# Kernel optimization log

Measured on AMD Instinct MI355X. Metric: run time of the kernel, lower is better.

Reference implementation:

```python
import jax, jax.numpy as jnp
import numpy as np

B, N, DIM, H, DH, M = 4, 1024, 1024, 16, 64, 16  # batch, seq, model dim, heads, head dim, num_mem_kv
QK_SCALE = 10.0  # qk_norm_scale


def l2norm(t, eps=1e-12):
    # F.normalize(t, dim=-1) with clamp_min(eps), groups=1
    n = jnp.linalg.norm(t, axis=-1, keepdims=True)
    return t / jnp.maximum(n, eps)


def rotate_half(x):
    # interleaved pairs: (x0,x1) -> (-x1, x0)
    x = x.reshape(*x.shape[:-1], -1, 2)
    x1, x2 = x[..., 0], x[..., 1]
    return jnp.stack((-x2, x1), axis=-1).reshape(*x.shape[:-2], x.shape[-2] * 2)


def apply_rope(t, freqs):
    # freqs: [n, d], t: [b, h, n, d]
    return t * jnp.cos(freqs) + rotate_half(t) * jnp.sin(freqs)


def setup_inputs() -> dict:
    key = jax.random.key(0)
    ks = jax.random.split(key, 14)
    x = jax.random.normal(ks[0], (B, N, DIM), dtype=jnp.float32)
    # rotary freqs: outer(pos, inv_freq) with each freq repeated twice (interleaved pairs)
    pos = jnp.arange(N, dtype=jnp.float32)
    inv_freq = 1.0 / (10000.0 ** (jnp.arange(0, DH, 2, dtype=jnp.float32) / DH))
    freqs = jnp.repeat(pos[:, None] * inv_freq[None, :], 2, axis=-1)  # [N, DH]
    s = 0.02
    Wq = jax.random.normal(ks[1], (DIM, H * DH), dtype=jnp.float32) * s
    Wk = jax.random.normal(ks[2], (DIM, H * DH), dtype=jnp.float32) * s
    Wv = jax.random.normal(ks[3], (DIM, H * DH), dtype=jnp.float32) * s
    q_scale = 1.0 + 0.1 * jax.random.normal(ks[4], (H, 1, DH), dtype=jnp.float32)
    k_scale = 1.0 + 0.1 * jax.random.normal(ks[5], (H, 1, DH), dtype=jnp.float32)
    mem_k = jax.random.normal(ks[6], (H, M, DH), dtype=jnp.float32)
    mem_v = jax.random.normal(ks[7], (H, M, DH), dtype=jnp.float32)
    W_pre = jnp.eye(H, dtype=jnp.float32) + 0.05 * jax.random.normal(ks[8], (H, H), dtype=jnp.float32)
    W_post = jnp.eye(H, dtype=jnp.float32) + 0.05 * jax.random.normal(ks[9], (H, H), dtype=jnp.float32)
    W_hgate = jax.random.normal(ks[10], (DIM, H), dtype=jnp.float32) * s
    b_hgate = jnp.full((H,), 2.0, dtype=jnp.float32)
    W_vgate = jax.random.normal(ks[11], (DIM, H * DH), dtype=jnp.float32) * s
    b_vgate = jnp.full((H * DH,), 2.0, dtype=jnp.float32)
    Wo = jax.random.normal(ks[12], (H * DH, DIM), dtype=jnp.float32) * s
    return dict(x=x, freqs=freqs, Wq=Wq, Wk=Wk, Wv=Wv, q_scale=q_scale, k_scale=k_scale,
                mem_k=mem_k, mem_v=mem_v, W_pre=W_pre, W_post=W_post,
                W_hgate=W_hgate, b_hgate=b_hgate, W_vgate=W_vgate, b_vgate=b_vgate, Wo=Wo)


def reference(x, freqs, Wq, Wk, Wv, q_scale, k_scale, mem_k, mem_v,
              W_pre, W_post, W_hgate, b_hgate, W_vgate, b_vgate, Wo):
    b, n, _ = x.shape
    # projections -> [b, h, n, dh]
    q = (x @ Wq).reshape(b, n, H, DH).transpose(0, 2, 1, 3)
    k = (x @ Wk).reshape(b, n, H, DH).transpose(0, 2, 1, 3)
    v = (x @ Wv).reshape(b, n, H, DH).transpose(0, 2, 1, 3)
    # qk l2-norm (groups=1) + learned per-head dim scales
    q = l2norm(q) * q_scale
    k = l2norm(k) * k_scale
    # rotary (xpos_scale = None -> scale 1)
    q = apply_rope(q, freqs)
    k = apply_rope(k, freqs)
    # memory key/values, prepended along the kv sequence axis
    mk = (l2norm(mem_k) * k_scale)[None].repeat(b, axis=0)  # [b,h,M,dh]
    mv = mem_v[None].repeat(b, axis=0)
    k = jnp.concatenate((mk, k), axis=-2)  # [b,h,M+n,dh]
    v = jnp.concatenate((mv, v), axis=-2)
    i, j = q.shape[-2], k.shape[-2]
    dots = jnp.einsum('bhid,bhjd->bhij', q, k) * QK_SCALE
    dots = jnp.einsum('bhij,gh->bgij', dots, W_pre)  # pre-softmax talking heads
    # causal mask (memory slots at the front are always visible)
    qpos = jnp.arange(i)
    kpos = jnp.arange(j)
    causal = kpos[None, :] > (qpos[:, None] + (j - i))  # True -> masked
    mask_value = -jnp.finfo(dots.dtype).max
    dots = jnp.where(causal[None, None], mask_value, dots)
    attn = jax.nn.softmax(dots, axis=-1)
    attn = jnp.einsum('bhij,gh->bgij', attn, W_post)  # post-softmax talking heads
    out = jnp.einsum('bhij,bhjd->bhid', attn, v)  # [b,h,n,dh]
    # per-head value gate
    head_gate = jax.nn.sigmoid(x @ W_hgate + b_hgate)  # [b,n,h]
    out = out * head_gate.transpose(0, 2, 1)[..., None]
    out = out.transpose(0, 2, 1, 3).reshape(b, n, H * DH)
    # per-dim value gate (sigmoid)
    out = out * jax.nn.sigmoid(x @ W_vgate + b_vgate)
    return out @ Wo
```

## Files before the change

### kernel.cpp

```cpp
#include <hip/hip_runtime.h>
#include <hip/hip_bf16.h>
#include <cmath>

typedef __attribute__((ext_vector_type(8))) short short8;
typedef __attribute__((ext_vector_type(4))) float f32x4;

__device__ __forceinline__ unsigned short to_bf(float f) {
  __hip_bfloat16 h = __float2bfloat16(f);
  return __builtin_bit_cast(unsigned short, h);
}

__global__ __launch_bounds__(256)
void cvt_bf16x4(const float* __restrict__ in, unsigned short* __restrict__ out, int n4)
{
  int i = blockIdx.x * 256 + threadIdx.x;
  if (i < n4) {
    float4 v = ((const float4*)in)[i];
    ushort4 o;
    o.x = to_bf(v.x); o.y = to_bf(v.y); o.z = to_bf(v.z); o.w = to_bf(v.w);
    ((ushort4*)out)[i] = o;
  }
}

__global__ __launch_bounds__(256)
void transpose_to_bf(const float* __restrict__ W, unsigned short* __restrict__ WT)
{
  __shared__ float tile[64][65];
  const int n0 = blockIdx.x * 64, k0 = blockIdx.y * 64;
  const int t = threadIdx.x, c = t & 63, r4 = t >> 6;
#pragma unroll
  for (int q = 0; q < 16; ++q) {
    int r = (q << 2) + r4;
    tile[r][c] = W[(size_t)(k0 + r) * 1024 + n0 + c];
  }
  __syncthreads();
#pragma unroll
  for (int q = 0; q < 16; ++q) {
    int r = (q << 2) + r4;
    WT[(size_t)(n0 + r) * 1024 + k0 + c] = to_bf(tile[c][r]);
  }
}

__global__ __launch_bounds__(256)
void gemm_bf128(const unsigned short* __restrict__ A, const unsigned short* __restrict__ BT,
                float* __restrict__ C, unsigned short* __restrict__ Vout,
                const float* __restrict__ bias2, int mode)
{
  __shared__ __align__(16) unsigned short Ab[128 * 40];
  __shared__ __align__(16) unsigned short Bb[128 * 40];
  const int t = threadIdx.x, lane = t & 63, w = t >> 6;
  const int m = lane & 15, quad = lane >> 4;
  const int wm = w & 1, wn = w >> 1;
  const int row0 = blockIdx.y << 7, col0 = blockIdx.x << 7;

  const int c0 = t,        r0 = c0 >> 2, kp0 = c0 & 3;
  const int c1 = t + 256,  r1 = c1 >> 2, kp1 = c1 & 3;

  f32x4 acc[4][4];
#pragma unroll
  for (int mi = 0; mi < 4; ++mi)
#pragma unroll
    for (int ni = 0; ni < 4; ++ni) acc[mi][ni] = (f32x4){0.f, 0.f, 0.f, 0.f};

  uint4 pa0 = *(const uint4*)(A + (size_t)(row0 + r0) * 1024 + kp0 * 8);
  uint4 pa1 = *(const uint4*)(A + (size_t)(row0 + r1) * 1024 + kp1 * 8);
  uint4 pb0 = *(const uint4*)(BT + (size_t)(col0 + r0) * 1024 + kp0 * 8);
  uint4 pb1 = *(const uint4*)(BT + (size_t)(col0 + r1) * 1024 + kp1 * 8);

  for (int kk = 0; kk < 1024; kk += 32) {
    *(uint4*)((char*)Ab + r0 * 80 + kp0 * 16) = pa0;
    *(uint4*)((char*)Ab + r1 * 80 + kp1 * 16) = pa1;
    *(uint4*)((char*)Bb + r0 * 80 + kp0 * 16) = pb0;
    *(uint4*)((char*)Bb + r1 * 80 + kp1 * 16) = pb1;
    __syncthreads();
    if (kk + 32 < 1024) {
      pa0 = *(const uint4*)(A + (size_t)(row0 + r0) * 1024 + kk + 32 + kp0 * 8);
      pa1 = *(const uint4*)(A + (size_t)(row0 + r1) * 1024 + kk + 32 + kp1 * 8);
      pb0 = *(const uint4*)(BT + (size_t)(col0 + r0) * 1024 + kk + 32 + kp0 * 8);
      pb1 = *(const uint4*)(BT + (size_t)(col0 + r1) * 1024 + kk + 32 + kp1 * 8);
    }
    short8 af[4], bf[4];
#pragma unroll
    for (int mi = 0; mi < 4; ++mi)
      af[mi] = *(const short8*)((char*)Ab + ((wm << 6) + (mi << 4) + m) * 80 + quad * 16);
#pragma unroll
    for (int ni = 0; ni < 4; ++ni)
      bf[ni] = *(const short8*)((char*)Bb + ((wn << 6) + (ni << 4) + m) * 80 + quad * 16);
#pragma unroll
    for (int mi = 0; mi < 4; ++mi)
#pragma unroll
      for (int ni = 0; ni < 4; ++ni)
        acc[mi][ni] = __builtin_amdgcn_mfma_f32_16x16x32_bf16(af[mi], bf[ni], acc[mi][ni], 0, 0, 0);
    __syncthreads();
  }
#pragma unroll
  for (int mi = 0; mi < 4; ++mi)
#pragma unroll
    for (int ni = 0; ni < 4; ++ni)
#pragma unroll
      for (int reg = 0; reg < 4; ++reg) {
        int mrow = row0 + (wm << 6) + (mi << 4) + (quad << 2) + reg;
        int ncol = col0 + (wn << 6) + (ni << 4) + m;
        float v = acc[mi][ni][reg];
        if (mode == 0) {
          C[((size_t)mrow << 10) + ncol] = v;
        } else if (mode == 2) {
          float s = v + bias2[ncol];
          C[((size_t)mrow << 10) + ncol] = 1.f / (1.f + __expf(-s));
        } else {
          int bb = mrow >> 10, nn = mrow & 1023;
          Vout[((size_t)((bb << 10) + ncol)) * 1056 + 16 + nn] = to_bf(v);
        }
      }
}

__global__ __launch_bounds__(256)
void hgate_proj(const float* __restrict__ x, const float* __restrict__ W,
                const float* __restrict__ bias, float* __restrict__ hg)
{
  int G = blockIdx.x * 256 + threadIdx.x;
  int row = G >> 4, h = G & 15;
  const float4* x4 = (const float4*)(x + ((size_t)row << 10));
  float acc = 0.f;
#pragma unroll 4
  for (int k4 = 0; k4 < 256; ++k4) {
    float4 xv = x4[k4];
    int kb = k4 << 2;
    acc += xv.x * W[(kb + 0) * 16 + h] + xv.y * W[(kb + 1) * 16 + h]
         + xv.z * W[(kb + 2) * 16 + h] + xv.w * W[(kb + 3) * 16 + h];
  }
  float v = acc + bias[h];
  hg[(row << 4) + h] = 1.f / (1.f + __expf(-v));
}

__global__ __launch_bounds__(256)
void q_post_bf(const float* __restrict__ q_lin, const float* __restrict__ scale,
               const float* __restrict__ freqs, unsigned short* __restrict__ qb)
{
  int gid = blockIdx.x * 256 + threadIdx.x;
  int d = gid & 63;
  int row = gid >> 6;
  int h = row & 15;
  int n = (row >> 4) & 1023;
  float v = q_lin[gid];
  float ss = v * v;
#pragma unroll
  for (int off = 32; off; off >>= 1) ss += __shfl_xor(ss, off);
  v = v / fmaxf(sqrtf(ss), 1e-12f) * scale[(h << 6) + d];
  float f = freqs[(n << 6) + d];
  float other = __shfl_xor(v, 1);
  float rot = (d & 1) ? other : -other;
  qb[gid] = to_bf((v * cosf(f) + rot * sinf(f)) * 10.f);
}

__global__ __launch_bounds__(256)
void k_post_bf(const float* __restrict__ k_lin, const float* __restrict__ scale,
               const float* __restrict__ freqs, unsigned short* __restrict__ kall)
{
  int gid = blockIdx.x * 256 + threadIdx.x;
  int d = gid & 63;
  int row = gid >> 6;
  int h = row & 15;
  int n = (row >> 4) & 1023;
  int b = row >> 14;
  float v = k_lin[gid];
  float ss = v * v;
#pragma unroll
  for (int off = 32; off; off >>= 1) ss += __shfl_xor(ss, off);
  v = v / fmaxf(sqrtf(ss), 1e-12f) * scale[(h << 6) + d];
  float f = freqs[(n << 6) + d];
  float other = __shfl_xor(v, 1);
  float rot = (d & 1) ? other : -other;
  float out = v * cosf(f) + rot * sinf(f);
  kall[(size_t)(b * 1056 + 16 + n) * 1024 + (h << 6) + d] = to_bf(out);
}

__global__ __launch_bounds__(256)
void mem_build(const float* __restrict__ mem_k, const float* __restrict__ mem_v,
               const float* __restrict__ k_scale,
               unsigned short* __restrict__ kall, unsigned short* __restrict__ vallT)
{
  int gid = blockIdx.x * 256 + threadIdx.x;
  int d = gid & 63;
  int row = gid >> 6;
  int h = row >> 4, mm = row & 15;
  float v = mem_k[gid];
  float ss = v * v;
#pragma unroll
  for (int off = 32; off; off >>= 1) ss += __shfl_xor(ss, off);
  unsigned short kb = to_bf(v / fmaxf(sqrtf(ss), 1e-12f) * k_scale[(h << 6) + d]);
  unsigned short vb = to_bf(mem_v[gid]);
#pragma unroll
  for (int b = 0; b < 4; ++b) {
    kall[(size_t)(b * 1056 + mm) * 1024 + (h << 6) + d] = kb;
    vallT[(size_t)((b << 10) + (h << 6) + d) * 1056 + mm] = vb;
  }
}


__global__ __launch_bounds__(256, 3)
void attn_lsum(const unsigned short* __restrict__ qb, const unsigned short* __restrict__ kall,
               const float* __restrict__ W_pre, float* __restrict__ Lbuf)
{
  __shared__ float sS[16 * 16 * 33];
  __shared__ f32x4 sWpre4[64];

  const int t = threadIdx.x, lane = t & 63, w = t >> 6;
  const int m = lane & 15, quad = lane >> 4;
  if (t < 64) {
    int h = t >> 2, p4 = t & 3;
    sWpre4[t] = (f32x4){W_pre[(4 * p4 + 0) * 16 + h], W_pre[(4 * p4 + 1) * 16 + h],
                        W_pre[(4 * p4 + 2) * 16 + h], W_pre[(4 * p4 + 3) * 16 + h]};
  }

  const int blk = blockIdx.x;
  const int u0 = (4352 * blk) >> 10, u1 = (4352 * (blk + 1)) >> 10;
  if (u0 == u1) return;

  int accu = 0, bi = 0;
  while (true) {
    int un = (((bi & 63) + 1) >> 1) + 1;
    if (accu + un > u0) break;
    accu += un; ++bi;
  }
  int b = bi >> 6, it = bi & 63, uoff = u0 - accu;

  short8 afr[4][2];
  float partL[16];
  bool fresh = true;

  for (int u = u0; u < u1; ++u) {
    const int i0 = it << 4;
    if (fresh) {
#pragma unroll
      for (int hh = 0; hh < 4; ++hh)
#pragma unroll
        for (int kk = 0; kk < 2; ++kk)
          afr[hh][kk] = *(const short8*)(qb + (((size_t)(b << 10) + i0 + m) << 10)
                                         + ((w << 2) + hh) * 64 + kk * 32 + quad * 8);
#pragma unroll
      for (int g = 0; g < 16; ++g) partL[g] = 0.f;
      fresh = false;
    }
    const int j0 = uoff << 5;
#pragma unroll
    for (int sub = 0; sub < 2; ++sub) {
      const int js = j0 + (sub << 4);
#pragma unroll
      for (int hh = 0; hh < 4; ++hh) {
        f32x4 s = (f32x4){0.f, 0.f, 0.f, 0.f};
#pragma unroll
        for (int kk = 0; kk < 2; ++kk) {
          short8 bfr = *(const short8*)(kall + ((size_t)(b * 1056 + js + m) << 10)
                                        + ((w << 2) + hh) * 64 + kk * 32 + quad * 8);
          s = __builtin_amdgcn_mfma_f32_16x16x32_bf16(afr[hh][kk], bfr, s, 0, 0, 0);
        }
#pragma unroll
        for (int reg = 0; reg < 4; ++reg)
          sS[(((w << 2) + hh) * 16 + (quad << 2) + reg) * 33 + (sub << 4) + m] = s[reg];
      }
    }
    __syncthreads();
    {
      const int i_l = t >> 4, j_l = t & 15;
      const int ig = i0 + i_l;
      float ch0[16], ch1[16];
#pragma unroll
      for (int h = 0; h < 16; ++h) {
        ch0[h] = sS[(h * 16 + i_l) * 33 + j_l];
        ch1[h] = sS[(h * 16 + i_l) * 33 + 16 + j_l];
      }
      f32x4 a0[4], a1[4];
#pragma unroll
      for (int p = 0; p < 4; ++p) { a0[p] = (f32x4){0.f,0.f,0.f,0.f}; a1[p] = a0[p]; }
#pragma unroll
      for (int h = 0; h < 16; ++h) {
        float c0 = ch0[h], c1 = ch1[h];
#pragma unroll
        for (int p = 0; p < 4; ++p) {
          f32x4 wv = sWpre4[(h << 2) + p];
          a0[p] += wv * c0;
          a1[p] += wv * c1;
        }
      }
      const bool ok0 = (j0 + j_l) <= ig + 16;
      const bool ok1 = (j0 + 16 + j_l) <= ig + 16;
#pragma unroll
      for (int p = 0; p < 4; ++p)
#pragma unroll
        for (int e = 0; e < 4; ++e) {
          float v0 = ok0 ? __expf(a0[p][e] - 20.f) : 0.f;
          float v1 = ok1 ? __expf(a1[p][e] - 20.f) : 0.f;
          partL[(p << 2) + e] += v0 + v1;
        }
    }
    __syncthreads();
    ++uoff;
    if (uoff == ((it + 1) >> 1) + 1) {
#pragma unroll
      for (int g = 0; g < 16; ++g) {
        float v = partL[g];
        v += __shfl_xor(v, 1); v += __shfl_xor(v, 2);
        v += __shfl_xor(v, 4); v += __shfl_xor(v, 8);
        if (m == 0)
          atomicAdd(&Lbuf[(((size_t)(b << 10) + i0 + (w << 2) + quad) << 4) + g], v);
      }
      ++bi; b = bi >> 6; it = bi & 63; uoff = 0; fresh = true;
    }
  }
  if (!fresh) {
    const int i0 = it << 4;
#pragma unroll
    for (int g = 0; g < 16; ++g) {
      float v = partL[g];
      v += __shfl_xor(v, 1); v += __shfl_xor(v, 2);
      v += __shfl_xor(v, 4); v += __shfl_xor(v, 8);
      if (m == 0)
        atomicAdd(&Lbuf[(((size_t)(b << 10) + i0 + (w << 2) + quad) << 4) + g], v);
    }
  }
}

__global__ __launch_bounds__(256)
void attn_pv2(const unsigned short* __restrict__ qb, const unsigned short* __restrict__ kall,
              const unsigned short* __restrict__ vallT, const float* __restrict__ W_pre,
              const float* __restrict__ W_post, const float* __restrict__ Lbuf,
              float* __restrict__ Obuf)
{
  __shared__ float sS[16 * 16 * 33];
  __shared__ unsigned short sE[16 * 16 * 40];
  __shared__ f32x4 sWpre4[64], sWpost4[64];
  __shared__ float sIL[256];

  const int t = threadIdx.x, lane = t & 63, w = t >> 6;
  const int m = lane & 15, quad = lane >> 4;
  if (t < 64) {
    int h = t >> 2, p4 = t & 3;
    sWpre4[t]  = (f32x4){W_pre[(4 * p4 + 0) * 16 + h],  W_pre[(4 * p4 + 1) * 16 + h],
                         W_pre[(4 * p4 + 2) * 16 + h],  W_pre[(4 * p4 + 3) * 16 + h]};
    sWpost4[t] = (f32x4){W_post[(4 * p4 + 0) * 16 + h], W_post[(4 * p4 + 1) * 16 + h],
                         W_post[(4 * p4 + 2) * 16 + h], W_post[(4 * p4 + 3) * 16 + h]};
  }

  const int blk = blockIdx.x;
  const int u0 = (4352 * blk) >> 9, u1 = (4352 * (blk + 1)) >> 9;
  if (u0 == u1) return;

  int accu = 0, bi = 0;
  while (true) {
    int un = (((bi & 63) + 1) >> 1) + 1;
    if (accu + un > u0) break;
    accu += un; ++bi;
  }
  int b = bi >> 6, it = bi & 63, uoff = u0 - accu;

  short8 afr[4][2];
  f32x4 oacc[4][4];
  bool fresh = true;

  for (int u = u0; u < u1; ++u) {
    const int i0 = it << 4;
    if (fresh) {
#pragma unroll
      for (int hh = 0; hh < 4; ++hh)
#pragma unroll
        for (int kk = 0; kk < 2; ++kk)
          afr[hh][kk] = *(const short8*)(qb + (((size_t)(b << 10) + i0 + m) << 10)
                                         + ((w << 2) + hh) * 64 + kk * 32 + quad * 8);
#pragma unroll
      for (int a = 0; a < 4; ++a)
#pragma unroll
        for (int dt = 0; dt < 4; ++dt) oacc[a][dt] = (f32x4){0.f, 0.f, 0.f, 0.f};
      sIL[t] = 1.f / Lbuf[(((size_t)(b << 10) + i0 + (t >> 4)) << 4) + (t & 15)];
      fresh = false;
    }
    const int j0 = uoff << 5;
#pragma unroll
    for (int sub = 0; sub < 2; ++sub) {
      const int js = j0 + (sub << 4);
#pragma unroll
      for (int hh = 0; hh < 4; ++hh) {
        f32x4 s = (f32x4){0.f, 0.f, 0.f, 0.f};
#pragma unroll
        for (int kk = 0; kk < 2; ++kk) {
          short8 bfr = *(const short8*)(kall + ((size_t)(b * 1056 + js + m) << 10)
                                        + ((w << 2) + hh) * 64 + kk * 32 + quad * 8);
          s = __builtin_amdgcn_mfma_f32_16x16x32_bf16(afr[hh][kk], bfr, s, 0, 0, 0);
        }
#pragma unroll
        for (int reg = 0; reg < 4; ++reg)
          sS[(((w << 2) + hh) * 16 + (quad << 2) + reg) * 33 + (sub << 4) + m] = s[reg];
      }
    }
    __syncthreads();
    {
      const int i_l = t >> 4, j_l = t & 15;
      const int ig = i0 + i_l;
      float ch0[16], ch1[16];
#pragma unroll
      for (int h = 0; h < 16; ++h) {
        ch0[h] = sS[(h * 16 + i_l) * 33 + j_l];
        ch1[h] = sS[(h * 16 + i_l) * 33 + 16 + j_l];
      }
      f32x4 a0[4], a1[4];
#pragma unroll
      for (int p = 0; p < 4; ++p) { a0[p] = (f32x4){0.f,0.f,0.f,0.f}; a1[p] = a0[p]; }
#pragma unroll
      for (int h = 0; h < 16; ++h) {
        float c0 = ch0[h], c1 = ch1[h];
#pragma unroll
        for (int p = 0; p < 4; ++p) {
          f32x4 wv = sWpre4[(h << 2) + p];
          a0[p] += wv * c0;
          a1[p] += wv * c1;
        }
      }
      const bool ok0 = (j0 + j_l) <= ig + 16;
      const bool ok1 = (j0 + 16 + j_l) <= ig + 16;
      float e0[16], e1[16];
#pragma unroll
      for (int p = 0; p < 4; ++p)
#pragma unroll
        for (int e = 0; e < 4; ++e) {
          int g = (p << 2) + e;
          float il = sIL[(i_l << 4) + g];
          e0[g] = ok0 ? __expf(a0[p][e] - 20.f) * il : 0.f;
          e1[g] = ok1 ? __expf(a1[p][e] - 20.f) * il : 0.f;
        }
      f32x4 b0[4], b1[4];
#pragma unroll
      for (int p = 0; p < 4; ++p) { b0[p] = (f32x4){0.f,0.f,0.f,0.f}; b1[p] = b0[p]; }
#pragma unroll
      for (int g = 0; g < 16; ++g) {
        float c0 = e0[g], c1 = e1[g];
#pragma unroll
        for (int p = 0; p < 4; ++p) {
          f32x4 wv = sWpost4[(g << 2) + p];
          b0[p] += wv * c0;
          b1[p] += wv * c1;
        }
      }
#pragma unroll
      for (int p = 0; p < 4; ++p)
#pragma unroll
        for (int e = 0; e < 4; ++e) {
          int g2 = (p << 2) + e;
          sE[(g2 * 16 + i_l) * 40 + j_l] = to_bf(b0[p][e]);
          sE[(g2 * 16 + i_l) * 40 + 16 + j_l] = to_bf(b1[p][e]);
        }
    }
    __syncthreads();
#pragma unroll
    for (int gl = 0; gl < 4; ++gl) {
      const int g2 = (w << 2) + gl;
      short8 a = *(const short8*)((const char*)sE + ((g2 * 16 + m) * 40 + quad * 8) * 2);
#pragma unroll
      for (int dt = 0; dt < 4; ++dt) {
        short8 bv = *(const short8*)(vallT + ((size_t)((b << 10) + g2 * 64 + dt * 16 + m)) * 1056
                                     + j0 + quad * 8);
        oacc[gl][dt] = __builtin_amdgcn_mfma_f32_16x16x32_bf16(a, bv, oacc[gl][dt], 0, 0, 0);
      }
    }
    ++uoff;
    if (uoff == ((it + 1) >> 1) + 1) {
#pragma unroll
      for (int gl = 0; gl < 4; ++gl) {
        int g2 = (w << 2) + gl;
#pragma unroll
        for (int dt = 0; dt < 4; ++dt)
#pragma unroll
          for (int reg = 0; reg < 4; ++reg)
            atomicAdd(&Obuf[(((size_t)(b << 10) + i0 + (quad << 2) + reg) << 10)
                            + g2 * 64 + dt * 16 + m], oacc[gl][dt][reg]);
      }
      ++bi; b = bi >> 6; it = bi & 63; uoff = 0; fresh = true;
    }
  }
  if (!fresh) {
    const int i0 = it << 4;
#pragma unroll
    for (int gl = 0; gl < 4; ++gl) {
      int g2 = (w << 2) + gl;
#pragma unroll
      for (int dt = 0; dt < 4; ++dt)
#pragma unroll
        for (int reg = 0; reg < 4; ++reg)
          atomicAdd(&Obuf[(((size_t)(b << 10) + i0 + (quad << 2) + reg) << 10)
                          + g2 * 64 + dt * 16 + m], oacc[gl][dt][reg]);
    }
  }
}

__global__ __launch_bounds__(256)
void gate_out(const float* __restrict__ Obuf, const float* __restrict__ hgate,
              const float* __restrict__ vgate, unsigned short* __restrict__ aob)
{
  int i4 = blockIdx.x * 256 + threadIdx.x;
  float4 o = ((const float4*)Obuf)[i4];
  int base = i4 << 2;
  int row = base >> 10, hd = base & 1023, h = hd >> 6;
  float hg = hgate[(row << 4) + h];
  float4 vg = ((const float4*)vgate)[i4];
  ushort4 r;
  r.x = to_bf(o.x * hg * vg.x);
  r.y = to_bf(o.y * hg * vg.y);
  r.z = to_bf(o.z * hg * vg.z);
  r.w = to_bf(o.w * hg * vg.w);
  ((ushort4*)aob)[i4] = r;
}

extern "C" void kernel_launch(void* const* d_in, const int* in_sizes, int n_in,
                              void* d_out, int out_size, void* d_ws, size_t ws_size,
                              hipStream_t stream)
{
  const float* x       = (const float*)d_in[0];
  const float* freqs   = (const float*)d_in[1];
  const float* Wq      = (const float*)d_in[2];
  const float* Wk      = (const float*)d_in[3];
  const float* Wv      = (const float*)d_in[4];
  const float* q_scale = (const float*)d_in[5];
  const float* k_scale = (const float*)d_in[6];
  const float* mem_k   = (const float*)d_in[7];
  const float* mem_v   = (const float*)d_in[8];
  const float* W_pre   = (const float*)d_in[9];
  const float* W_post  = (const float*)d_in[10];
  const float* W_hg    = (const float*)d_in[11];
  const float* b_hg    = (const float*)d_in[12];
  const float* W_vg    = (const float*)d_in[13];
  const float* b_vg    = (const float*)d_in[14];
  const float* Wo      = (const float*)d_in[15];
  float* out = (float*)d_out;
  float* ws  = (float*)d_ws;

  float* q_lin = ws;
  unsigned short* aob = (unsigned short*)ws;
  float* Lbuf  = ws + 4128768;
  float* k_lin = ws + 4194304;
  float* Obuf  = k_lin;
  float* vgbuf = ws + 8388608;
  float* hgbuf = ws + 12582912;
  unsigned short* xb   = (unsigned short*)(ws + 12713984);
  unsigned short* qb   = xb;
  unsigned short* kall = (unsigned short*)(ws + 14811136);
  unsigned short* vallT= (unsigned short*)(ws + 16973824);
  unsigned short* wb   = (unsigned short*)(ws + 19136512);

  dim3 blk(256);
  cvt_bf16x4<<<4096, blk, 0, stream>>>(x, xb, 1048576);
  hgate_proj<<<256, blk, 0, stream>>>(x, W_hg, b_hg, hgbuf);
  transpose_to_bf<<<dim3(16, 16), blk, 0, stream>>>(Wq, wb);
  gemm_bf128<<<dim3(8, 32), blk, 0, stream>>>(xb, wb, q_lin, nullptr, nullptr, 0);
  transpose_to_bf<<<dim3(16, 16), blk, 0, stream>>>(Wk, wb);
  gemm_bf128<<<dim3(8, 32), blk, 0, stream>>>(xb, wb, k_lin, nullptr, nullptr, 0);
  transpose_to_bf<<<dim3(16, 16), blk, 0, stream>>>(Wv, wb);
  gemm_bf128<<<dim3(8, 32), blk, 0, stream>>>(xb, wb, nullptr, vallT, nullptr, 1);
  transpose_to_bf<<<dim3(16, 16), blk, 0, stream>>>(W_vg, wb);
  gemm_bf128<<<dim3(8, 32), blk, 0, stream>>>(xb, wb, vgbuf, nullptr, b_vg, 2);
  q_post_bf<<<16384, blk, 0, stream>>>(q_lin, q_scale, freqs, qb);
  k_post_bf<<<16384, blk, 0, stream>>>(k_lin, k_scale, freqs, kall);
  mem_build<<<64, blk, 0, stream>>>(mem_k, mem_v, k_scale, kall, vallT);
  hipMemsetAsync(Lbuf, 0, (65536 + 4194304) * sizeof(float), stream);
  attn_lsum<<<1024, blk, 0, stream>>>(qb, kall, W_pre, Lbuf);
  attn_pv2<<<512, blk, 0, stream>>>(qb, kall, vallT, W_pre, W_post, Lbuf, Obuf);
  gate_out<<<4096, blk, 0, stream>>>(Obuf, hgbuf, vgbuf, aob);
  transpose_to_bf<<<dim3(16, 16), blk, 0, stream>>>(Wo, wb);
  gemm_bf128<<<dim3(8, 32), blk, 0, stream>>>(aob, wb, out, nullptr, nullptr, 0);
}
```

Baseline: 558.3 us.

## Restructure attention kernels so each wave owns key columns across all heads

Both attention kernels now give each wave 16 key columns across all 16 heads, so the talking-heads mixing runs in registers on the MFMA outputs. This removes the fp32 score staging through shared memory and one barrier per step. Key tiles grow from 32 to 64 columns, with a fixed number of work units per block (2 for lsum, 5 for pv) and adjusted grid sizes. In exchange, Q fragments are reloaded from global memory per unit rather than kept in registers, register pressure rises (pv2 now has a 3-blocks-per-SM bound), and the last key tile needs clamped indexing.

```diff
diff --git a/kernel.cpp b/kernel.cpp
--- a/kernel.cpp
+++ b/kernel.cpp
@@ -202,9 +202,7 @@
 void attn_lsum(const unsigned short* __restrict__ qb, const unsigned short* __restrict__ kall,
                const float* __restrict__ W_pre, float* __restrict__ Lbuf)
 {
-  __shared__ float sS[16 * 16 * 33];
   __shared__ f32x4 sWpre4[64];
-
   const int t = threadIdx.x, lane = t & 63, w = t >> 6;
   const int m = lane & 15, quad = lane >> 4;
   if (t < 64) {
@@ -212,123 +210,111 @@
     sWpre4[t] = (f32x4){W_pre[(4 * p4 + 0) * 16 + h], W_pre[(4 * p4 + 1) * 16 + h],
                         W_pre[(4 * p4 + 2) * 16 + h], W_pre[(4 * p4 + 3) * 16 + h]};
   }
-
-  const int blk = blockIdx.x;
-  const int u0 = (4352 * blk) >> 10, u1 = (4352 * (blk + 1)) >> 10;
-  if (u0 == u1) return;
+  __syncthreads();
+
+  int u = 2 * blockIdx.x;
+  const int u1 = u + 2;
 
   int accu = 0, bi = 0;
   while (true) {
-    int un = (((bi & 63) + 1) >> 1) + 1;
-    if (accu + un > u0) break;
+    int un = ((bi & 63) + 5) >> 2;
+    if (accu + un > u) break;
     accu += un; ++bi;
   }
-  int b = bi >> 6, it = bi & 63, uoff = u0 - accu;
-
-  short8 afr[4][2];
-  float partL[16];
+  int b = bi >> 6, it = bi & 63, uoff = u - accu;
+
+  f32x4 partL[4][4];
   bool fresh = true;
 
-  for (int u = u0; u < u1; ++u) {
+  for (; u < u1; ++u) {
     const int i0 = it << 4;
     if (fresh) {
 #pragma unroll
-      for (int hh = 0; hh < 4; ++hh)
-#pragma unroll
-        for (int kk = 0; kk < 2; ++kk)
-          afr[hh][kk] = *(const short8*)(qb + (((size_t)(b << 10) + i0 + m) << 10)
-                                         + ((w << 2) + hh) * 64 + kk * 32 + quad * 8);
-#pragma unroll
-      for (int g = 0; g < 16; ++g) partL[g] = 0.f;
+      for (int r = 0; r < 4; ++r)
+#pragma unroll
+        for (int p = 0; p < 4; ++p) partL[r][p] = (f32x4){0.f, 0.f, 0.f, 0.f};
       fresh = false;
     }
-    const int j0 = uoff << 5;
-#pragma unroll
-    for (int sub = 0; sub < 2; ++sub) {
-      const int js = j0 + (sub << 4);
-#pragma unroll
-      for (int hh = 0; hh < 4; ++hh) {
-        f32x4 s = (f32x4){0.f, 0.f, 0.f, 0.f};
-#pragma unroll
-        for (int kk = 0; kk < 2; ++kk) {
-          short8 bfr = *(const short8*)(kall + ((size_t)(b * 1056 + js + m) << 10)
-                                        + ((w << 2) + hh) * 64 + kk * 32 + quad * 8);
-          s = __builtin_amdgcn_mfma_f32_16x16x32_bf16(afr[hh][kk], bfr, s, 0, 0, 0);
-        }
-#pragma unroll
-        for (int reg = 0; reg < 4; ++reg)
-          sS[(((w << 2) + hh) * 16 + (quad << 2) + reg) * 33 + (sub << 4) + m] = s[reg];
-      }
-    }
-    __syncthreads();
-    {
-      const int i_l = t >> 4, j_l = t & 15;
-      const int ig = i0 + i_l;
-      float ch0[16], ch1[16];
+    const int js = (uoff << 6) + (w << 4);
+    if (js <= i0 + 31) {
+      const int jj = min(js + m, 1055);
+      const unsigned short* qrow = qb + (((size_t)((b << 10) + i0 + m)) << 10);
+      const unsigned short* krow = kall + (((size_t)(b * 1056 + jj)) << 10);
+      f32x4 ap[4][4];
+#pragma unroll
+      for (int r = 0; r < 4; ++r)
+#pragma unroll
+        for (int p = 0; p < 4; ++p) ap[r][p] = (f32x4){0.f, 0.f, 0.f, 0.f};
 #pragma unroll
       for (int h = 0; h < 16; ++h) {
-        ch0[h] = sS[(h * 16 + i_l) * 33 + j_l];
-        ch1[h] = sS[(h * 16 + i_l) * 33 + 16 + j_l];
-      }
-      f32x4 a0[4], a1[4];
-#pragma unroll
-      for (int p = 0; p < 4; ++p) { a0[p] = (f32x4){0.f,0.f,0.f,0.f}; a1[p] = a0[p]; }
-#pragma unroll
-      for (int h = 0; h < 16; ++h) {
-        float c0 = ch0[h], c1 = ch1[h];
+        short8 q0 = *(const short8*)(qrow + h * 64 + quad * 8);
+        short8 q1 = *(const short8*)(qrow + h * 64 + 32 + quad * 8);
+        short8 k0 = *(const short8*)(krow + h * 64 + quad * 8);
+        short8 k1 = *(const short8*)(krow + h * 64 + 32 + quad * 8);
+        f32x4 acc = (f32x4){0.f, 0.f, 0.f, 0.f};
+        acc = __builtin_amdgcn_mfma_f32_16x16x32_bf16(q0, k0, acc, 0, 0, 0);
+        acc = __builtin_amdgcn_mfma_f32_16x16x32_bf16(q1, k1, acc, 0, 0, 0);
 #pragma unroll
         for (int p = 0; p < 4; ++p) {
           f32x4 wv = sWpre4[(h << 2) + p];
-          a0[p] += wv * c0;
-          a1[p] += wv * c1;
+#pragma unroll
+          for (int r = 0; r < 4; ++r) ap[r][p] += wv * acc[r];
         }
       }
-      const bool ok0 = (j0 + j_l) <= ig + 16;
-      const bool ok1 = (j0 + 16 + j_l) <= ig + 16;
-#pragma unroll
-      for (int p = 0; p < 4; ++p)
-#pragma unroll
-        for (int e = 0; e < 4; ++e) {
-          float v0 = ok0 ? __expf(a0[p][e] - 20.f) : 0.f;
-          float v1 = ok1 ? __expf(a1[p][e] - 20.f) : 0.f;
-          partL[(p << 2) + e] += v0 + v1;
-        }
-    }
-    __syncthreads();
+#pragma unroll
+      for (int r = 0; r < 4; ++r) {
+        const int iL = (quad << 2) + r;
+        const bool ok = (js + m) <= (i0 + iL + 16);
+#pragma unroll
+        for (int p = 0; p < 4; ++p)
+#pragma unroll
+          for (int e = 0; e < 4; ++e)
+            partL[r][p][e] += ok ? __expf(ap[r][p][e] - 20.f) : 0.f;
+      }
+    }
     ++uoff;
-    if (uoff == ((it + 1) >> 1) + 1) {
-#pragma unroll
-      for (int g = 0; g < 16; ++g) {
-        float v = partL[g];
-        v += __shfl_xor(v, 1); v += __shfl_xor(v, 2);
-        v += __shfl_xor(v, 4); v += __shfl_xor(v, 8);
-        if (m == 0)
-          atomicAdd(&Lbuf[(((size_t)(b << 10) + i0 + (w << 2) + quad) << 4) + g], v);
-      }
+    if (uoff == ((it + 5) >> 2)) {
+#pragma unroll
+      for (int r = 0; r < 4; ++r)
+#pragma unroll
+        for (int p = 0; p < 4; ++p)
+#pragma unroll
+          for (int e = 0; e < 4; ++e) {
+            float v = partL[r][p][e];
+            v += __shfl_xor(v, 1); v += __shfl_xor(v, 2);
+            v += __shfl_xor(v, 4); v += __shfl_xor(v, 8);
+            if (m == 0)
+              atomicAdd(&Lbuf[(((size_t)(b << 10) + i0 + (quad << 2) + r) << 4)
+                              + (p << 2) + e], v);
+          }
       ++bi; b = bi >> 6; it = bi & 63; uoff = 0; fresh = true;
     }
   }
   if (!fresh) {
     const int i0 = it << 4;
 #pragma unroll
-    for (int g = 0; g < 16; ++g) {
-      float v = partL[g];
-      v += __shfl_xor(v, 1); v += __shfl_xor(v, 2);
-      v += __shfl_xor(v, 4); v += __shfl_xor(v, 8);
-      if (m == 0)
-        atomicAdd(&Lbuf[(((size_t)(b << 10) + i0 + (w << 2) + quad) << 4) + g], v);
-    }
-  }
-}
-
-__global__ __launch_bounds__(256)
+    for (int r = 0; r < 4; ++r)
+#pragma unroll
+      for (int p = 0; p < 4; ++p)
+#pragma unroll
+        for (int e = 0; e < 4; ++e) {
+          float v = partL[r][p][e];
+          v += __shfl_xor(v, 1); v += __shfl_xor(v, 2);
+          v += __shfl_xor(v, 4); v += __shfl_xor(v, 8);
+          if (m == 0)
+            atomicAdd(&Lbuf[(((size_t)(b << 10) + i0 + (quad << 2) + r) << 4)
+                            + (p << 2) + e], v);
+        }
+  }
+}
+
+__global__ __launch_bounds__(256, 3)
 void attn_pv2(const unsigned short* __restrict__ qb, const unsigned short* __restrict__ kall,
               const unsigned short* __restrict__ vallT, const float* __restrict__ W_pre,
               const float* __restrict__ W_post, const float* __restrict__ Lbuf,
               float* __restrict__ Obuf)
 {
-  __shared__ float sS[16 * 16 * 33];
-  __shared__ unsigned short sE[16 * 16 * 40];
+  __shared__ unsigned short sE[16 * 16 * 76];
   __shared__ f32x4 sWpre4[64], sWpost4[64];
   __shared__ float sIL[256];
 
@@ -341,128 +327,111 @@
     sWpost4[t] = (f32x4){W_post[(4 * p4 + 0) * 16 + h], W_post[(4 * p4 + 1) * 16 + h],
                          W_post[(4 * p4 + 2) * 16 + h], W_post[(4 * p4 + 3) * 16 + h]};
   }
-
-  const int blk = blockIdx.x;
-  const int u0 = (4352 * blk) >> 9, u1 = (4352 * (blk + 1)) >> 9;
-  if (u0 == u1) return;
+  __syncthreads();
+
+  int u = 5 * blockIdx.x;
+  const int u1 = u + 5;
 
   int accu = 0, bi = 0;
   while (true) {
-    int un = (((bi & 63) + 1) >> 1) + 1;
-    if (accu + un > u0) break;
+    int un = ((bi & 63) + 5) >> 2;
+    if (accu + un > u) break;
     accu += un; ++bi;
   }
-  int b = bi >> 6, it = bi & 63, uoff = u0 - accu;
-
-  short8 afr[4][2];
+  int b = bi >> 6, it = bi & 63, uoff = u - accu;
+
   f32x4 oacc[4][4];
   bool fresh = true;
 
-  for (int u = u0; u < u1; ++u) {
+  for (; u < u1; ++u) {
     const int i0 = it << 4;
     if (fresh) {
-#pragma unroll
-      for (int hh = 0; hh < 4; ++hh)
-#pragma unroll
-        for (int kk = 0; kk < 2; ++kk)
-          afr[hh][kk] = *(const short8*)(qb + (((size_t)(b << 10) + i0 + m) << 10)
-                                         + ((w << 2) + hh) * 64 + kk * 32 + quad * 8);
 #pragma unroll
       for (int a = 0; a < 4; ++a)
 #pragma unroll
         for (int dt = 0; dt < 4; ++dt) oacc[a][dt] = (f32x4){0.f, 0.f, 0.f, 0.f};
       sIL[t] = 1.f / Lbuf[(((size_t)(b << 10) + i0 + (t >> 4)) << 4) + (t & 15)];
       fresh = false;
-    }
-    const int j0 = uoff << 5;
-#pragma unroll
-    for (int sub = 0; sub < 2; ++sub) {
-      const int js = j0 + (sub << 4);
-#pragma unroll
-      for (int hh = 0; hh < 4; ++hh) {
-        f32x4 s = (f32x4){0.f, 0.f, 0.f, 0.f};
-#pragma unroll
-        for (int kk = 0; kk < 2; ++kk) {
-          short8 bfr = *(const short8*)(kall + ((size_t)(b * 1056 + js + m) << 10)
-                                        + ((w << 2) + hh) * 64 + kk * 32 + quad * 8);
-          s = __builtin_amdgcn_mfma_f32_16x16x32_bf16(afr[hh][kk], bfr, s, 0, 0, 0);
+      __syncthreads();
+    }
+    const int j0 = uoff << 6;
+    const int js = j0 + (w << 4);
+    const int jj = min(js + m, 1055);
+    const unsigned short* qrow = qb + (((size_t)((b << 10) + i0 + m)) << 10);
+    const unsigned short* krow = kall + (((size_t)(b * 1056 + jj)) << 10);
+
+    f32x4 ap[4][4];
+#pragma unroll
+    for (int r = 0; r < 4; ++r)
+#pragma unroll
+      for (int p = 0; p < 4; ++p) ap[r][p] = (f32x4){0.f, 0.f, 0.f, 0.f};
+#pragma unroll
+    for (int h = 0; h < 16; ++h) {
+      short8 q0 = *(const short8*)(qrow + h * 64 + quad * 8);
+      short8 q1 = *(const short8*)(qrow + h * 64 + 32 + quad * 8);
+      short8 k0 = *(const short8*)(krow + h * 64 + quad * 8);
+      short8 k1 = *(const short8*)(krow + h * 64 + 32 + quad * 8);
+      f32x4 acc = (f32x4){0.f, 0.f, 0.f, 0.f};
+      acc = __builtin_amdgcn_mfma_f32_16x16x32_bf16(q0, k0, acc, 0, 0, 0);
+      acc = __builtin_amdgcn_mfma_f32_16x16x32_bf16(q1, k1, acc, 0, 0, 0);
+#pragma unroll
+      for (int p = 0; p < 4; ++p) {
+        f32x4 wv = sWpre4[(h << 2) + p];
+#pragma unroll
+        for (int r = 0; r < 4; ++r) ap[r][p] += wv * acc[r];
+      }
+    }
+#pragma unroll
+    for (int r = 0; r < 4; ++r) {
+      const int iL = (quad << 2) + r;
+      const bool ok = (js + m) <= (i0 + iL + 16);
+#pragma unroll
+      for (int p = 0; p < 4; ++p)
+#pragma unroll
+        for (int e = 0; e < 4; ++e) {
+          float il = sIL[(iL << 4) + (p << 2) + e];
+          ap[r][p][e] = ok ? __expf(ap[r][p][e] - 20.f) * il : 0.f;
         }
-#pragma unroll
-        for (int reg = 0; reg < 4; ++reg)
-          sS[(((w << 2) + hh) * 16 + (quad << 2) + reg) * 33 + (sub << 4) + m] = s[reg];
-      }
-    }
-    __syncthreads();
-    {
-      const int i_l = t >> 4, j_l = t & 15;
-      const int ig = i0 + i_l;
-      float ch0[16], ch1[16];
-#pragma unroll
-      for (int h = 0; h < 16; ++h) {
-        ch0[h] = sS[(h * 16 + i_l) * 33 + j_l];
-        ch1[h] = sS[(h * 16 + i_l) * 33 + 16 + j_l];
-      }
-      f32x4 a0[4], a1[4];
-#pragma unroll
-      for (int p = 0; p < 4; ++p) { a0[p] = (f32x4){0.f,0.f,0.f,0.f}; a1[p] = a0[p]; }
-#pragma unroll
-      for (int h = 0; h < 16; ++h) {
-        float c0 = ch0[h], c1 = ch1[h];
-#pragma unroll
-        for (int p = 0; p < 4; ++p) {
-          f32x4 wv = sWpre4[(h << 2) + p];
-          a0[p] += wv * c0;
-          a1[p] += wv * c1;
-        }
-      }
-      const bool ok0 = (j0 + j_l) <= ig + 16;
-      const bool ok1 = (j0 + 16 + j_l) <= ig + 16;
-      float e0[16], e1[16];
-#pragma unroll
-      for (int p = 0; p < 4; ++p)
-#pragma unroll
-        for (int e = 0; e < 4; ++e) {
-          int g = (p << 2) + e;
-          float il = sIL[(i_l << 4) + g];
-          e0[g] = ok0 ? __expf(a0[p][e] - 20.f) * il : 0.f;
-          e1[g] = ok1 ? __expf(a1[p][e] - 20.f) * il : 0.f;
-        }
-      f32x4 b0[4], b1[4];
-#pragma unroll
-      for (int p = 0; p < 4; ++p) { b0[p] = (f32x4){0.f,0.f,0.f,0.f}; b1[p] = b0[p]; }
+    }
+#pragma unroll
+    for (int q = 0; q < 4; ++q) {
+      f32x4 bp[4];
+#pragma unroll
+      for (int r = 0; r < 4; ++r) bp[r] = (f32x4){0.f, 0.f, 0.f, 0.f};
 #pragma unroll
       for (int g = 0; g < 16; ++g) {
-        float c0 = e0[g], c1 = e1[g];
-#pragma unroll
-        for (int p = 0; p < 4; ++p) {
-          f32x4 wv = sWpost4[(g << 2) + p];
-          b0[p] += wv * c0;
-          b1[p] += wv * c1;
-        }
-      }
-#pragma unroll
-      for (int p = 0; p < 4; ++p)
-#pragma unroll
-        for (int e = 0; e < 4; ++e) {
-          int g2 = (p << 2) + e;
-          sE[(g2 * 16 + i_l) * 40 + j_l] = to_bf(b0[p][e]);
-          sE[(g2 * 16 + i_l) * 40 + 16 + j_l] = to_bf(b1[p][e]);
-        }
+        f32x4 wv = sWpost4[(g << 2) + q];
+#pragma unroll
+        for (int r = 0; r < 4; ++r) bp[r] += wv * ap[r][g >> 2][g & 3];
+      }
+#pragma unroll
+      for (int r = 0; r < 4; ++r) {
+        const int iL = (quad << 2) + r;
+#pragma unroll
+        for (int e2 = 0; e2 < 4; ++e2)
+          sE[(((q << 2) + e2) * 16 + iL) * 76 + (w << 4) + m] = to_bf(bp[r][e2]);
+      }
     }
     __syncthreads();
 #pragma unroll
     for (int gl = 0; gl < 4; ++gl) {
       const int g2 = (w << 2) + gl;
-      short8 a = *(const short8*)((const char*)sE + ((g2 * 16 + m) * 40 + quad * 8) * 2);
+      short8 a0 = *(const short8*)(sE + (g2 * 16 + m) * 76 + quad * 8);
+      short8 a1 = *(const short8*)(sE + (g2 * 16 + m) * 76 + 32 + quad * 8);
 #pragma unroll
       for (int dt = 0; dt < 4; ++dt) {
-        short8 bv = *(const short8*)(vallT + ((size_t)((b << 10) + g2 * 64 + dt * 16 + m)) * 1056
-                                     + j0 + quad * 8);
-        oacc[gl][dt] = __builtin_amdgcn_mfma_f32_16x16x32_bf16(a, bv, oacc[gl][dt], 0, 0, 0);
-      }
-    }
+        const size_t vrow = ((size_t)((b << 10) + g2 * 64 + dt * 16 + m)) * 1056;
+        const int c0 = min(j0 + quad * 8, 1048);
+        const int c1 = min(j0 + 32 + quad * 8, 1048);
+        short8 v0 = *(const short8*)(vallT + vrow + c0);
+        short8 v1 = *(const short8*)(vallT + vrow + c1);
+        oacc[gl][dt] = __builtin_amdgcn_mfma_f32_16x16x32_bf16(a0, v0, oacc[gl][dt], 0, 0, 0);
+        oacc[gl][dt] = __builtin_amdgcn_mfma_f32_16x16x32_bf16(a1, v1, oacc[gl][dt], 0, 0, 0);
+      }
+    }
+    __syncthreads();
     ++uoff;
-    if (uoff == ((it + 1) >> 1) + 1) {
+    if (uoff == ((it + 5) >> 2)) {
 #pragma unroll
       for (int gl = 0; gl < 4; ++gl) {
         int g2 = (w << 2) + gl;
@@ -560,8 +529,8 @@
   k_post_bf<<<16384, blk, 0, stream>>>(k_lin, k_scale, freqs, kall);
   mem_build<<<64, blk, 0, stream>>>(mem_k, mem_v, k_scale, kall, vallT);
   hipMemsetAsync(Lbuf, 0, (65536 + 4194304) * sizeof(float), stream);
-  attn_lsum<<<1024, blk, 0, stream>>>(qb, kall, W_pre, Lbuf);
-  attn_pv2<<<512, blk, 0, stream>>>(qb, kall, vallT, W_pre, W_post, Lbuf, Obuf);
+  attn_lsum<<<1120, blk, 0, stream>>>(qb, kall, W_pre, Lbuf);
+  attn_pv2<<<448, blk, 0, stream>>>(qb, kall, vallT, W_pre, W_post, Lbuf, Obuf);
   gate_out<<<4096, blk, 0, stream>>>(Obuf, hgbuf, vgbuf, aob);
   transpose_to_bf<<<dim3(16, 16), blk, 0, stream>>>(Wo, wb);
   gemm_bf128<<<dim3(8, 32), blk, 0, stream>>>(aob, wb, out, nullptr, nullptr, 0);
```

Result: slower. 1.626 ms (+191.3%).
